# Kernel tuning notes

Measured on AMD Instinct MI355X. Metric: run time of the kernel, lower is better.

## Reference

```python
import jax, jax.numpy as jnp
import numpy as np

BIG = 1e9  # self-distance masking constant, as in the torch module


def setup_inputs() -> dict:
    key = jax.random.key(0)
    k1, _ = jax.random.split(key)
    coords = jax.random.normal(k1, (8, 4096, 3), dtype=jnp.float32)
    mask = jnp.ones((8, 4096), dtype=bool)
    return {"coords": coords, "mask": mask}


def reference(coords, mask):
    # coords: [B, N, 3]; mask is accepted but unused (matches the torch module)
    B, N, _ = coords.shape
    # Pairwise Euclidean distances via the |a|^2 + |b|^2 - 2ab identity
    # (avoids materializing the [B,N,N,3] diff tensor the torch code builds).
    sq = jnp.sum(coords * coords, axis=-1)                      # [B, N]
    inner = jnp.einsum('bnd,bmd->bnm', coords, coords)          # [B, N, N]
    d2 = sq[:, :, None] + sq[:, None, :] - 2.0 * inner
    dist = jnp.sqrt(jnp.maximum(d2, 0.0))                       # [B, N, N]
    dist = dist + jnp.eye(N, dtype=dist.dtype) * BIG            # mask self
    # argsort(dim=2)[:, :, :2] == indices of the two smallest distances
    _, idx = jax.lax.top_k(-dist, 2)                            # [B, N, 2]
    first_nearest_indices = idx[:, :, 0]
    second_nearest_indices = idx[:, :, 1]
    A = jnp.take_along_axis(
        coords, jnp.broadcast_to(first_nearest_indices[:, :, None], (B, N, 3)), axis=1)
    C = jnp.take_along_axis(
        coords, jnp.broadcast_to(second_nearest_indices[:, :, None], (B, N, 3)), axis=1)
    return (A, C, first_nearest_indices, second_nearest_indices)
```

## Files before the change

### kernel.cpp

```cpp
#include <hip/hip_runtime.h>

#define BATCH 8
#define NPTS 4096
#define TOTQ (BATCH * NPTS)
#define TPB 256
#define BIGD 1e30f

__device__ __forceinline__ float cand_w(float x, float y, float z) {
    return fmaf(x, x, fmaf(y, y, z * z));
}
__device__ __forceinline__ float cand_key(float cx, float cy, float cz, float w,
                                          float xn, float yn, float zn) {
    return fmaf(cx, xn, fmaf(cy, yn, fmaf(cz, zn, w)));
}

__device__ __forceinline__ void top2min(float k, int m,
                                        float& b1, int& i1,
                                        float& b2, int& i2) {
    bool c1 = k < b1;
    bool c2 = k < b2;
    int ni2 = c2 ? m : i2;
    i2 = c1 ? i1 : ni2;
    i1 = c1 ? m : i1;
    b2 = fminf(fmaxf(k, b1), b2);
    b1 = fminf(k, b1);
}

template <int NCHUNKS, int Q>
__global__ __launch_bounds__(TPB, 4) void knn_scan(const float* __restrict__ coords,
                                                   float2* __restrict__ partial) {
    constexpr int CHUNKSZ = NPTS / NCHUNKS;
    __shared__ float4 pts[CHUNKSZ];
    const int tid   = (int)threadIdx.x;
    const int tile  = blockIdx.x;
    const int chunk = blockIdx.y;
    const int b     = blockIdx.z;
    const float* basep = coords + (size_t)b * NPTS * 3;
    const int mbase = chunk * CHUNKSZ;

    for (int p = tid; p < CHUNKSZ; p += TPB) {
        float x = basep[(mbase + p) * 3 + 0];
        float y = basep[(mbase + p) * 3 + 1];
        float z = basep[(mbase + p) * 3 + 2];
        pts[p] = make_float4(-2.0f * x, -2.0f * y, -2.0f * z, cand_w(x, y, z));
    }

    const int qbase = tile * (TPB * Q);
    float xn[Q], yn[Q], zn[Q], b1[Q], b2[Q];
#pragma unroll
    for (int q = 0; q < Q; ++q) {
        int n = qbase + q * TPB + tid;
        xn[q] = basep[n * 3 + 0];
        yn[q] = basep[n * 3 + 1];
        zn[q] = basep[n * 3 + 2];
        b1[q] = BIGD; b2[q] = BIGD;
    }
    __syncthreads();

    for (int p = 0; p < CHUNKSZ; p += 8) {
        float4 c[8];
#pragma unroll
        for (int j = 0; j < 8; ++j) c[j] = pts[p + j];
#pragma unroll
        for (int j = 0; j < 8; ++j) {
#pragma unroll
            for (int q = 0; q < Q; ++q) {
                float k = cand_key(c[j].x, c[j].y, c[j].z, c[j].w, xn[q], yn[q], zn[q]);
                b2[q] = fminf(fmaxf(k, b1[q]), b2[q]);
                b1[q] = fminf(k, b1[q]);
            }
        }
    }

#pragma unroll
    for (int q = 0; q < Q; ++q) {
        int n = qbase + q * TPB + tid;
        partial[(size_t)chunk * TOTQ + (size_t)b * NPTS + n] = make_float2(b1[q], b2[q]);
    }
}

template <int CHUNKSZ>
__device__ __forceinline__ void rescan_chunk(const float* __restrict__ basep, int c, int n,
                                             float xn, float yn, float zn,
                                             float& r1, int& j1, float& r2, int& j2) {
    r1 = BIGD; r2 = BIGD; j1 = 0; j2 = 0;
    const int m0 = c * CHUNKSZ;
    for (int m = m0; m < m0 + CHUNKSZ; ++m) {
        float x = basep[m * 3 + 0];
        float y = basep[m * 3 + 1];
        float z = basep[m * 3 + 2];
        float w = cand_w(x, y, z);
        float k = cand_key(-2.0f * x, -2.0f * y, -2.0f * z, w, xn, yn, zn);
        k = (m == n) ? BIGD : k;
        top2min(k, m, r1, j1, r2, j2);
    }
}

template <int NCHUNKS>
__global__ __launch_bounds__(TPB) void knn_merge(const float* __restrict__ coords,
                                                 const float2* __restrict__ partial,
                                                 float* __restrict__ out) {
    constexpr int CHUNKSZ = NPTS / NCHUNKS;
    const int q = blockIdx.x * TPB + (int)threadIdx.x;
    const int b = q >> 12;
    const int n = q & (NPTS - 1);
    const float* basep = coords + (size_t)b * NPTS * 3;
    const int c_self = n / CHUNKSZ;

    const float xn = basep[n * 3 + 0];
    const float yn = basep[n * 3 + 1];
    const float zn = basep[n * 3 + 2];

    float v1 = BIGD, v2 = BIGD;
    int ca = (c_self == 0) ? 1 : 0, cbk = ca;
    for (int c = 0; c < NCHUNKS; ++c) {
        if (c == c_self) continue;
        float2 v = partial[(size_t)c * TOTQ + q];
        top2min(v.x, c, v1, ca, v2, cbk);
        top2min(v.y, c, v1, ca, v2, cbk);
    }

    int lo3 = min(min(c_self, ca), cbk);
    int hi3 = max(max(c_self, ca), cbk);
    int md3 = c_self + ca + cbk - lo3 - hi3;

    float f1 = BIGD, f2 = BIGD;
    int g1 = 0, g2 = 0;
    float r1, r2; int j1, j2;

    rescan_chunk<CHUNKSZ>(basep, lo3, n, xn, yn, zn, r1, j1, r2, j2);
    top2min(r1, j1, f1, g1, f2, g2);
    top2min(r2, j2, f1, g1, f2, g2);
    if (md3 > lo3) {
        rescan_chunk<CHUNKSZ>(basep, md3, n, xn, yn, zn, r1, j1, r2, j2);
        top2min(r1, j1, f1, g1, f2, g2);
        top2min(r2, j2, f1, g1, f2, g2);
    }
    if (hi3 > md3) {
        rescan_chunk<CHUNKSZ>(basep, hi3, n, xn, yn, zn, r1, j1, r2, j2);
        top2min(r1, j1, f1, g1, f2, g2);
        top2min(r2, j2, f1, g1, f2, g2);
    }

    float* A  = out;
    float* C  = out + (size_t)TOTQ * 3;
    float* I1 = out + (size_t)2 * TOTQ * 3;
    float* I2 = I1 + (size_t)TOTQ;

    A[(size_t)q * 3 + 0] = basep[g1 * 3 + 0];
    A[(size_t)q * 3 + 1] = basep[g1 * 3 + 1];
    A[(size_t)q * 3 + 2] = basep[g1 * 3 + 2];
    C[(size_t)q * 3 + 0] = basep[g2 * 3 + 0];
    C[(size_t)q * 3 + 1] = basep[g2 * 3 + 1];
    C[(size_t)q * 3 + 2] = basep[g2 * 3 + 2];
    I1[q] = (float)g1;
    I2[q] = (float)g2;
}

__global__ __launch_bounds__(TPB) void knn_full(const float* __restrict__ coords,
                                                float* __restrict__ out) {
    __shared__ float4 pts[NPTS];
    const int tid  = (int)threadIdx.x;
    const int tile = blockIdx.x;
    const int b    = blockIdx.y;
    const float* basep = coords + (size_t)b * NPTS * 3;

    for (int p = tid; p < NPTS; p += TPB) {
        float x = basep[p * 3 + 0];
        float y = basep[p * 3 + 1];
        float z = basep[p * 3 + 2];
        pts[p] = make_float4(-2.0f * x, -2.0f * y, -2.0f * z, cand_w(x, y, z));
    }
    const int n = tile * TPB + tid;
    const float xn = basep[n * 3 + 0];
    const float yn = basep[n * 3 + 1];
    const float zn = basep[n * 3 + 2];
    __syncthreads();

    float b1 = BIGD, b2 = BIGD;
    int i1 = 0, i2 = 0;
    for (int p = 0; p < NPTS; p += 4) {
#pragma unroll
        for (int j = 0; j < 4; ++j) {
            float4 c = pts[p + j];
            float k = cand_key(c.x, c.y, c.z, c.w, xn, yn, zn);
            k = (p + j == n) ? BIGD : k;
            top2min(k, p + j, b1, i1, b2, i2);
        }
    }

    const int q = b * NPTS + n;
    float* A  = out;
    float* C  = out + (size_t)TOTQ * 3;
    float* I1 = out + (size_t)2 * TOTQ * 3;
    float* I2 = I1 + (size_t)TOTQ;
    float4 p1 = pts[i1];
    float4 p2 = pts[i2];
    A[(size_t)q * 3 + 0] = -0.5f * p1.x;
    A[(size_t)q * 3 + 1] = -0.5f * p1.y;
    A[(size_t)q * 3 + 2] = -0.5f * p1.z;
    C[(size_t)q * 3 + 0] = -0.5f * p2.x;
    C[(size_t)q * 3 + 1] = -0.5f * p2.y;
    C[(size_t)q * 3 + 2] = -0.5f * p2.z;
    I1[q] = (float)i1;
    I2[q] = (float)i2;
}

extern "C" void kernel_launch(void* const* d_in, const int* in_sizes, int n_in,
                              void* d_out, int out_size, void* d_ws, size_t ws_size,
                              hipStream_t stream) {
    const float* coords = (const float*)d_in[0];
    float* out = (float*)d_out;
    float2* partial = (float2*)d_ws;
    const size_t chunk_bytes = (size_t)TOTQ * sizeof(float2);

    if (ws_size >= 64 * chunk_bytes) {
        hipLaunchKernelGGL((knn_scan<64, 8>), dim3(2, 64, BATCH), dim3(TPB), 0, stream,
                           coords, partial);
        hipLaunchKernelGGL((knn_merge<64>), dim3(TOTQ / TPB), dim3(TPB), 0, stream,
                           coords, partial, out);
    } else if (ws_size >= 32 * chunk_bytes) {
        hipLaunchKernelGGL((knn_scan<32, 8>), dim3(2, 32, BATCH), dim3(TPB), 0, stream,
                           coords, partial);
        hipLaunchKernelGGL((knn_merge<32>), dim3(TOTQ / TPB), dim3(TPB), 0, stream,
                           coords, partial, out);
    } else if (ws_size >= 16 * chunk_bytes) {
        hipLaunchKernelGGL((knn_scan<16, 4>), dim3(4, 16, BATCH), dim3(TPB), 0, stream,
                           coords, partial);
        hipLaunchKernelGGL((knn_merge<16>), dim3(TOTQ / TPB), dim3(TPB), 0, stream,
                           coords, partial, out);
    } else {
        hipLaunchKernelGGL(knn_full, dim3(NPTS / TPB, BATCH), dim3(TPB), 0, stream,
                           coords, out);
    }
}
```

Before: 117.1 us.

## Track nearest index in scan to avoid rescanning winning chunks in merge

The scan kernel now records the argmin index per chunk alongside the top-2 values, stored in a separate workspace array. The merge picks the global top-2 across chunk slots and reads the stored index when a winner is a chunk's first minimum. It rescans a chunk only when a winner is that chunk's second minimum, and always rescans the query's own chunk. This cuts the common rescans from up to three chunks to about one, at the price of an extra select per candidate in the hot scan loop, more workspace traffic, a larger workspace requirement and a dropped 16-chunk path.

```diff
diff --git a/kernel.cpp b/kernel.cpp
--- a/kernel.cpp
+++ b/kernel.cpp
@@ -26,9 +26,23 @@
     b1 = fminf(k, b1);
 }
 
+__device__ __forceinline__ void top2lex(float k, int m,
+                                        float& b1, int& i1,
+                                        float& b2, int& i2) {
+    bool c1 = (k < b1) || (k == b1 && m < i1);
+    bool c2 = (k < b2) || (k == b2 && m < i2);
+    float nb2 = c1 ? b1 : (c2 ? k : b2);
+    int   ni2 = c1 ? i1 : (c2 ? m : i2);
+    b1 = c1 ? k : b1;
+    i1 = c1 ? m : i1;
+    b2 = nb2;
+    i2 = ni2;
+}
+
 template <int NCHUNKS, int Q>
 __global__ __launch_bounds__(TPB, 4) void knn_scan(const float* __restrict__ coords,
-                                                   float2* __restrict__ partial) {
+                                                   float2* __restrict__ vals,
+                                                   int* __restrict__ idx1) {
     constexpr int CHUNKSZ = NPTS / NCHUNKS;
     __shared__ float4 pts[CHUNKSZ];
     const int tid   = (int)threadIdx.x;
@@ -47,13 +61,14 @@
 
     const int qbase = tile * (TPB * Q);
     float xn[Q], yn[Q], zn[Q], b1[Q], b2[Q];
+    int i1[Q];
 #pragma unroll
     for (int q = 0; q < Q; ++q) {
         int n = qbase + q * TPB + tid;
         xn[q] = basep[n * 3 + 0];
         yn[q] = basep[n * 3 + 1];
         zn[q] = basep[n * 3 + 2];
-        b1[q] = BIGD; b2[q] = BIGD;
+        b1[q] = BIGD; b2[q] = BIGD; i1[q] = 0;
     }
     __syncthreads();
 
@@ -63,9 +78,12 @@
         for (int j = 0; j < 8; ++j) c[j] = pts[p + j];
 #pragma unroll
         for (int j = 0; j < 8; ++j) {
+            const int m = mbase + p + j;
 #pragma unroll
             for (int q = 0; q < Q; ++q) {
                 float k = cand_key(c[j].x, c[j].y, c[j].z, c[j].w, xn[q], yn[q], zn[q]);
+                bool c1 = k < b1[q];
+                i1[q] = c1 ? m : i1[q];
                 b2[q] = fminf(fmaxf(k, b1[q]), b2[q]);
                 b1[q] = fminf(k, b1[q]);
             }
@@ -74,15 +92,16 @@
 
 #pragma unroll
     for (int q = 0; q < Q; ++q) {
-        int n = qbase + q * TPB + tid;
-        partial[(size_t)chunk * TOTQ + (size_t)b * NPTS + n] = make_float2(b1[q], b2[q]);
+        int gq = (size_t)0 + b * NPTS + qbase + q * TPB + tid;
+        vals[(size_t)chunk * TOTQ + gq] = make_float2(b1[q], b2[q]);
+        idx1[(size_t)chunk * TOTQ + gq] = i1[q];
     }
 }
 
 template <int CHUNKSZ>
-__device__ __forceinline__ void rescan_chunk(const float* __restrict__ basep, int c, int n,
-                                             float xn, float yn, float zn,
-                                             float& r1, int& j1, float& r2, int& j2) {
+__device__ __forceinline__ void rescan_global(const float* __restrict__ basep, int c, int n,
+                                              float xn, float yn, float zn,
+                                              float& r1, int& j1, float& r2, int& j2) {
     r1 = BIGD; r2 = BIGD; j1 = 0; j2 = 0;
     const int m0 = c * CHUNKSZ;
     for (int m = m0; m < m0 + CHUNKSZ; ++m) {
@@ -98,7 +117,8 @@
 
 template <int NCHUNKS>
 __global__ __launch_bounds__(TPB) void knn_merge(const float* __restrict__ coords,
-                                                 const float2* __restrict__ partial,
+                                                 const float2* __restrict__ vals,
+                                                 const int* __restrict__ idx1,
                                                  float* __restrict__ out) {
     constexpr int CHUNKSZ = NPTS / NCHUNKS;
     const int q = blockIdx.x * TPB + (int)threadIdx.x;
@@ -111,50 +131,56 @@
     const float yn = basep[n * 3 + 1];
     const float zn = basep[n * 3 + 2];
 
-    float v1 = BIGD, v2 = BIGD;
-    int ca = (c_self == 0) ? 1 : 0, cbk = ca;
+    float f1 = BIGD, f2 = BIGD;
+    int ta = 0, tb = 0;
+#pragma unroll 8
     for (int c = 0; c < NCHUNKS; ++c) {
         if (c == c_self) continue;
-        float2 v = partial[(size_t)c * TOTQ + q];
-        top2min(v.x, c, v1, ca, v2, cbk);
-        top2min(v.y, c, v1, ca, v2, cbk);
-    }
-
-    int lo3 = min(min(c_self, ca), cbk);
-    int hi3 = max(max(c_self, ca), cbk);
-    int md3 = c_self + ca + cbk - lo3 - hi3;
-
-    float f1 = BIGD, f2 = BIGD;
-    int g1 = 0, g2 = 0;
+        float2 v = vals[(size_t)c * TOTQ + q];
+        top2min(v.x, 2 * c + 0, f1, ta, f2, tb);
+        top2min(v.y, 2 * c + 1, f1, ta, f2, tb);
+    }
+    const int ct1 = ta >> 1, s1 = ta & 1;
+    const int ct2 = tb >> 1, s2 = tb & 1;
+
     float r1, r2; int j1, j2;
-
-    rescan_chunk<CHUNKSZ>(basep, lo3, n, xn, yn, zn, r1, j1, r2, j2);
-    top2min(r1, j1, f1, g1, f2, g2);
-    top2min(r2, j2, f1, g1, f2, g2);
-    if (md3 > lo3) {
-        rescan_chunk<CHUNKSZ>(basep, md3, n, xn, yn, zn, r1, j1, r2, j2);
-        top2min(r1, j1, f1, g1, f2, g2);
-        top2min(r2, j2, f1, g1, f2, g2);
-    }
-    if (hi3 > md3) {
-        rescan_chunk<CHUNKSZ>(basep, hi3, n, xn, yn, zn, r1, j1, r2, j2);
-        top2min(r1, j1, f1, g1, f2, g2);
-        top2min(r2, j2, f1, g1, f2, g2);
-    }
+    int g1, g2;
+    if (s1 == 0) {
+        g1 = idx1[(size_t)ct1 * TOTQ + q];
+    } else {
+        rescan_global<CHUNKSZ>(basep, ct1, n, xn, yn, zn, r1, j1, r2, j2);
+        g1 = j2;
+    }
+    if (s2 == 0) {
+        g2 = idx1[(size_t)ct2 * TOTQ + q];
+    } else {
+        rescan_global<CHUNKSZ>(basep, ct2, n, xn, yn, zn, r1, j1, r2, j2);
+        g2 = j2;
+    }
+
+    float rs1, rs2; int js1, js2;
+    rescan_global<CHUNKSZ>(basep, c_self, n, xn, yn, zn, rs1, js1, rs2, js2);
+
+    float o1 = BIGD, o2 = BIGD;
+    int h1 = 0x7fffffff, h2 = 0x7fffffff;
+    top2lex(f1, g1, o1, h1, o2, h2);
+    top2lex(f2, g2, o1, h1, o2, h2);
+    top2lex(rs1, js1, o1, h1, o2, h2);
+    top2lex(rs2, js2, o1, h1, o2, h2);
 
     float* A  = out;
     float* C  = out + (size_t)TOTQ * 3;
     float* I1 = out + (size_t)2 * TOTQ * 3;
     float* I2 = I1 + (size_t)TOTQ;
 
-    A[(size_t)q * 3 + 0] = basep[g1 * 3 + 0];
-    A[(size_t)q * 3 + 1] = basep[g1 * 3 + 1];
-    A[(size_t)q * 3 + 2] = basep[g1 * 3 + 2];
-    C[(size_t)q * 3 + 0] = basep[g2 * 3 + 0];
-    C[(size_t)q * 3 + 1] = basep[g2 * 3 + 1];
-    C[(size_t)q * 3 + 2] = basep[g2 * 3 + 2];
-    I1[q] = (float)g1;
-    I2[q] = (float)g2;
+    A[(size_t)q * 3 + 0] = basep[h1 * 3 + 0];
+    A[(size_t)q * 3 + 1] = basep[h1 * 3 + 1];
+    A[(size_t)q * 3 + 2] = basep[h1 * 3 + 2];
+    C[(size_t)q * 3 + 0] = basep[h2 * 3 + 0];
+    C[(size_t)q * 3 + 1] = basep[h2 * 3 + 1];
+    C[(size_t)q * 3 + 2] = basep[h2 * 3 + 2];
+    I1[q] = (float)h1;
+    I2[q] = (float)h2;
 }
 
 __global__ __launch_bounds__(TPB) void knn_full(const float* __restrict__ coords,
@@ -211,24 +237,21 @@
                               hipStream_t stream) {
     const float* coords = (const float*)d_in[0];
     float* out = (float*)d_out;
-    float2* partial = (float2*)d_ws;
-    const size_t chunk_bytes = (size_t)TOTQ * sizeof(float2);
-
-    if (ws_size >= 64 * chunk_bytes) {
+
+    if (ws_size >= (size_t)64 * TOTQ * (sizeof(float2) + sizeof(int))) {
+        float2* vals = (float2*)d_ws;
+        int* idx1 = (int*)((char*)d_ws + (size_t)64 * TOTQ * sizeof(float2));
         hipLaunchKernelGGL((knn_scan<64, 8>), dim3(2, 64, BATCH), dim3(TPB), 0, stream,
-                           coords, partial);
+                           coords, vals, idx1);
         hipLaunchKernelGGL((knn_merge<64>), dim3(TOTQ / TPB), dim3(TPB), 0, stream,
-                           coords, partial, out);
-    } else if (ws_size >= 32 * chunk_bytes) {
+                           coords, vals, idx1, out);
+    } else if (ws_size >= (size_t)32 * TOTQ * (sizeof(float2) + sizeof(int))) {
+        float2* vals = (float2*)d_ws;
+        int* idx1 = (int*)((char*)d_ws + (size_t)32 * TOTQ * sizeof(float2));
         hipLaunchKernelGGL((knn_scan<32, 8>), dim3(2, 32, BATCH), dim3(TPB), 0, stream,
-                           coords, partial);
+                           coords, vals, idx1);
         hipLaunchKernelGGL((knn_merge<32>), dim3(TOTQ / TPB), dim3(TPB), 0, stream,
-                           coords, partial, out);
-    } else if (ws_size >= 16 * chunk_bytes) {
-        hipLaunchKernelGGL((knn_scan<16, 4>), dim3(4, 16, BATCH), dim3(TPB), 0, stream,
-                           coords, partial);
-        hipLaunchKernelGGL((knn_merge<16>), dim3(TOTQ / TPB), dim3(TPB), 0, stream,
-                           coords, partial, out);
+                           coords, vals, idx1, out);
     } else {
         hipLaunchKernelGGL(knn_full, dim3(NPTS / TPB, BATCH), dim3(TPB), 0, stream,
                            coords, out);
```

Result: no change. 118.4 us (+1.1%).
